# Optimization experiments

Hardware: AMD Instinct MI355X
Metric: run time of the kernel (lower is better)

Reference implementation:

```python
import jax, jax.numpy as jnp
import numpy as np

DIM = 384
HEADS = 12
HEAD_DIM = DIM // HEADS
WS = 8
SHIFT = 4
HID = int(DIM * 4.0)
N = WS * WS
EPS = 1e-5
NEG = -1e9


def _rel_index(ws):
    coords = np.stack(np.meshgrid(np.arange(ws), np.arange(ws), indexing='ij')).reshape(2, -1)
    rel = (coords[:, :, None] - coords[:, None, :]).transpose(1, 2, 0)
    rel[:, :, 0] += ws - 1
    rel[:, :, 1] += ws - 1
    return (rel[:, :, 0] * (2 * ws - 1) + rel[:, :, 1]).astype(np.int32)

REL_IDX = _rel_index(WS)  # [N, N]


def _shift_mask(H, W, ws, shift):
    img = np.zeros((H, W))
    cnt = 0
    sl = (slice(0, -ws), slice(-ws, -shift), slice(-shift, None))
    for h in sl:
        for w in sl:
            img[h, w] = cnt
            cnt += 1
    m = img.reshape(H // ws, ws, W // ws, ws).transpose(0, 2, 1, 3).reshape(-1, ws * ws)
    diff = m[:, :, None] - m[:, None, :]
    return np.where(diff != 0, NEG, 0.0).astype(np.float32)  # [nW, N, N]


def _ln(x, g, b):
    mu = jnp.mean(x, axis=-1, keepdims=True)
    var = jnp.mean(jnp.square(x - mu), axis=-1, keepdims=True)
    return (x - mu) * jax.lax.rsqrt(var + EPS) * g + b


def _l2norm(x):
    n = jnp.sqrt(jnp.sum(jnp.square(x), axis=-1, keepdims=True))
    return x / jnp.maximum(n, 1e-12)


def setup_inputs() -> dict:
    key = jax.random.key(0)
    ks = jax.random.split(key, 12)
    s = 0.02
    return {
        'x': jax.random.normal(ks[0], (16, 4096, DIM), jnp.float32),
        'H': 64,
        'W': 64,
        'norm_attn_g': jnp.ones((DIM,), jnp.float32),
        'norm_attn_b': jnp.zeros((DIM,), jnp.float32),
        'qkv_w': jax.random.normal(ks[1], (DIM, 3 * DIM), jnp.float32) * s,
        'qkv_b': jnp.zeros((3 * DIM,), jnp.float32),
        'proj_w': jax.random.normal(ks[2], (DIM, DIM), jnp.float32) * s,
        'proj_b': jnp.zeros((DIM,), jnp.float32),
        'tau': jnp.full((HEADS,), 0.07, jnp.float32),
        'rpb_table': jax.random.normal(ks[3], ((2 * WS - 1) ** 2, HEADS), jnp.float32) * s,
        'norm_mlp_g': jnp.ones((DIM,), jnp.float32),
        'norm_mlp_b': jnp.zeros((DIM,), jnp.float32),
        'fc1_w': jax.random.normal(ks[4], (DIM, HID), jnp.float32) * s,
        'fc1_b': jnp.zeros((HID,), jnp.float32),
        'fc2_w': jax.random.normal(ks[5], (HID, DIM), jnp.float32) * s,
        'fc2_b': jnp.zeros((DIM,), jnp.float32),
    }


def reference(x, H, W, norm_attn_g, norm_attn_b, qkv_w, qkv_b, proj_w, proj_b, tau,
              rpb_table, norm_mlp_g, norm_mlp_b, fc1_w, fc1_b, fc2_w, fc2_b):
    B, L, C = x.shape
    ws = WS
    nW = (H // ws) * (W // ws)
    mask = jnp.asarray(_shift_mask(H, W, ws, SHIFT))  # [nW, N, N], static

    shortcut = x
    xn = _ln(x, norm_attn_g, norm_attn_b).reshape(B, H, W, C)
    xn = jnp.roll(xn, (-SHIFT, -SHIFT), axis=(1, 2))
    # window partition -> [B*nW, N, C]
    win = xn.reshape(B, H // ws, ws, W // ws, ws, C).transpose(0, 1, 3, 2, 4, 5).reshape(-1, N, C)
    BnW = win.shape[0]

    qkv = (win @ qkv_w + qkv_b).reshape(BnW, N, 3, HEADS, HEAD_DIM)
    q = _l2norm(qkv[:, :, 0])  # [BnW, N, H, D]
    k = _l2norm(qkv[:, :, 1])
    v = qkv[:, :, 2]

    attn = jnp.einsum('bnhd,bmhd->bhnm', q, k)
    attn = attn / jnp.clip(tau, 0.001)[None, :, None, None]
    bias = rpb_table[REL_IDX.reshape(-1)].reshape(N, N, HEADS).transpose(2, 0, 1)  # [H, N, N]
    attn = attn + bias[None]
    attn = attn.reshape(B, nW, HEADS, N, N) + mask[None, :, None]
    attn = jax.nn.softmax(attn.reshape(BnW, HEADS, N, N), axis=-1)

    out = jnp.einsum('bhnm,bmhd->bnhd', attn, v).reshape(BnW, N, C)
    out = out @ proj_w + proj_b
    # window unpartition
    out = out.reshape(B, H // ws, W // ws, ws, ws, C).transpose(0, 1, 3, 2, 4, 5).reshape(B, H, W, C)
    out = jnp.roll(out, (SHIFT, SHIFT), axis=(1, 2)).reshape(B, L, C)

    x = shortcut + out
    xn2 = _ln(x, norm_mlp_g, norm_mlp_b)
    mlp = jax.nn.gelu(xn2 @ fc1_w + fc1_b, approximate=False) @ fc2_w + fc2_b
    return x + mlp
```

## Files before the change

### kernel.cpp

```cpp
#include <hip/hip_runtime.h>
#include <hip/hip_bf16.h>
#include <cstdint>

#define DIM     384
#define NHEADS  12
#define HD      32
#define HGRID   64
#define NTOK    64
#define MTOT    65536
#define HID     1536

typedef __attribute__((ext_vector_type(8))) short bf16x8;
typedef __attribute__((ext_vector_type(4))) float f32x4;
typedef __hip_bfloat16 bf16;

typedef __attribute__((address_space(1))) const void* as1_cvp;
typedef __attribute__((address_space(3))) void*       as3_vp;
#define GLDS16(g, l) __builtin_amdgcn_global_load_lds((as1_cvp)(g), (as3_vp)(l), 16, 0, 0)

__device__ __forceinline__ float bf2f(short s) {
  union { unsigned int u; float f; } x;
  x.u = ((unsigned int)(unsigned short)s) << 16;
  return x.f;
}
__device__ __forceinline__ unsigned int f2u(float f) {
  union { bf16 b; unsigned short s; } c;
  c.b = __float2bfloat16(f);
  return (unsigned int)c.s;
}

__global__ void wconv_kernel(const float* __restrict__ src, bf16* __restrict__ dst,
                             int K, int N) {
  int i = blockIdx.x * 256 + threadIdx.x;
  if (i >= K * N) return;
  int n = i / K, k = i - n * K;
  dst[i] = __float2bfloat16(src[(size_t)k * N + n]);
}

__global__ __launch_bounds__(384) void ln_kernel(const float* __restrict__ x,
    const float* __restrict__ g, const float* __restrict__ bta,
    bf16* __restrict__ out, int windowed) {
  const int row = blockIdx.x;
  const int c = threadIdx.x;
  size_t src;
  if (windowed) {
    int wg = row >> 6, n = row & 63;
    int b = wg >> 6, wi = wg & 63;
    int hp = ((wi >> 3) << 3) + (n >> 3);
    int wp = ((wi & 7) << 3) + (n & 7);
    int h = (hp + 4) & 63, w = (wp + 4) & 63;
    src = ((size_t)b * 4096 + h * 64 + w) * DIM;
  } else {
    src = (size_t)row * DIM;
  }
  float v = x[src + c];
  float s = v, ss = v * v;
  #pragma unroll
  for (int off = 32; off; off >>= 1) {
    s  += __shfl_xor(s,  off, 64);
    ss += __shfl_xor(ss, off, 64);
  }
  __shared__ float red[12];
  const int wave = threadIdx.x >> 6, lane = threadIdx.x & 63;
  if (lane == 0) { red[wave] = s; red[6 + wave] = ss; }
  __syncthreads();
  if (threadIdx.x == 0) {
    float ts = 0.f, tss = 0.f;
    #pragma unroll
    for (int i = 0; i < 6; i++) { ts += red[i]; tss += red[6 + i]; }
    red[0] = ts; red[6] = tss;
  }
  __syncthreads();
  const float mean = red[0] * (1.0f / DIM);
  const float var  = red[6] * (1.0f / DIM) - mean * mean;
  const float inv  = rsqrtf(var + 1e-5f);
  out[(size_t)row * DIM + c] = __float2bfloat16((v - mean) * inv * g[c] + bta[c]);
}

template <int EPI>
__global__ __launch_bounds__(512) void gemm_bt(
    const bf16* __restrict__ A, const bf16* __restrict__ Bt,
    const float* __restrict__ bias,
    bf16* __restrict__ outb, float* __restrict__ outf,
    const float* __restrict__ resid,
    int M, int N, int K, int gridN)
{
  __shared__ bf16 As[2][128 * 64];
  __shared__ bf16 Bs[2][128 * 64];
  const int tid = threadIdx.x;
  const int wave = tid >> 6, lane = tid & 63;

  const int bid = blockIdx.x;
  const int xcd = bid & 7, slot = bid >> 3;
  const int n_blk = slot % gridN;
  const int m_blk = (slot / gridN) * 8 + xcd;
  const int m0 = m_blk * 128, n0 = n_blk * 128;

  f32x4 acc[4][2];
  #pragma unroll
  for (int i = 0; i < 4; i++)
    #pragma unroll
    for (int j = 0; j < 2; j++) acc[i][j] = (f32x4){0.f, 0.f, 0.f, 0.f};

  const int q = lane >> 4, r = lane & 15;
  const int mwav = (wave >> 2) * 64;
  const int nwav = (wave & 3) * 32;

  const int srow = wave * 16 + (lane >> 3);
  const int gchunk = (lane & 7) ^ ((lane >> 3) & 7);
  const char* Ac = (const char*)A + (size_t)(m0 + srow) * K * 2 + gchunk * 16;
  const char* Bc = (const char*)Bt + (size_t)(n0 + srow) * K * 2 + gchunk * 16;
  const size_t rowskip8 = (size_t)8 * K * 2;
  const int ldsbase = wave * 16 * 64;

  const int rxor = r & 7;
  const int nt = K >> 6;

  {
    bf16* Ad = &As[0][ldsbase];
    bf16* Bd = &Bs[0][ldsbase];
    GLDS16(Ac,            Ad + 0 * 64);
    GLDS16(Ac + rowskip8, Ad + 8 * 64);
    GLDS16(Bc,            Bd + 0 * 64);
    GLDS16(Bc + rowskip8, Bd + 8 * 64);
  }

  int cur = 0;
  for (int t = 0; t < nt; ++t) {
    if (t + 1 < nt) {
      const size_t kb = (size_t)(t + 1) * 128;
      bf16* Ad = &As[cur ^ 1][ldsbase];
      bf16* Bd = &Bs[cur ^ 1][ldsbase];
      GLDS16(Ac + kb,            Ad + 0 * 64);
      GLDS16(Ac + kb + rowskip8, Ad + 8 * 64);
      GLDS16(Bc + kb,            Bd + 0 * 64);
      GLDS16(Bc + kb + rowskip8, Bd + 8 * 64);
      asm volatile("s_waitcnt vmcnt(4)" ::: "memory");
    } else {
      asm volatile("s_waitcnt vmcnt(0)" ::: "memory");
    }
    __builtin_amdgcn_sched_barrier(0);
    __builtin_amdgcn_s_barrier();

    const bf16* Ar = As[cur];
    const bf16* Br = Bs[cur];
    #pragma unroll
    for (int hh = 0; hh < 2; hh++) {
      const int s = (hh * 4 + q) ^ rxor;
      bf16x8 af[4], bfr[2];
      #pragma unroll
      for (int mi = 0; mi < 4; mi++)
        af[mi] = *(const bf16x8*)(&Ar[(mwav + mi * 16 + r) * 64 + s * 8]);
      #pragma unroll
      for (int ni = 0; ni < 2; ni++)
        bfr[ni] = *(const bf16x8*)(&Br[(nwav + ni * 16 + r) * 64 + s * 8]);
      #pragma unroll
      for (int mi = 0; mi < 4; mi++)
        #pragma unroll
        for (int ni = 0; ni < 2; ni++)
          acc[mi][ni] = __builtin_amdgcn_mfma_f32_16x16x32_bf16(af[mi], bfr[ni], acc[mi][ni], 0, 0, 0);
    }

    __builtin_amdgcn_s_barrier();
    cur ^= 1;
  }

  #pragma unroll
  for (int mi = 0; mi < 4; mi++) {
    #pragma unroll
    for (int ni = 0; ni < 2; ni++) {
      #pragma unroll
      for (int rr = 0; rr < 4; rr++) {
        const int row = m0 + mwav + mi * 16 + q * 4 + rr;
        const int col = n0 + nwav + ni * 16 + r;
        float val = acc[mi][ni][rr] + bias[col];
        if (EPI == 0) {
          outb[(size_t)row * N + col] = __float2bfloat16(val);
        } else if (EPI == 1) {
          const float t = val * val;
          const float z = val * fmaf(t, 0.07135481283f, 1.5957691216f);
          const float gl = val / (1.0f + __expf(-z));
          outb[(size_t)row * N + col] = __float2bfloat16(gl);
        } else if (EPI == 2) {
          const int wg = row >> 6, n = row & 63;
          const int b = wg >> 6, wi = wg & 63;
          const int hp = ((wi >> 3) << 3) + (n >> 3);
          const int wp = ((wi & 7) << 3) + (n & 7);
          const int h = (hp + 4) & 63, w = (wp + 4) & 63;
          const size_t dst = ((size_t)b * 4096 + h * 64 + w) * DIM + col;
          outf[dst] = resid[dst] + val;
        } else {
          outf[(size_t)row * N + col] += val;
        }
      }
    }
  }
}

__device__ __forceinline__ int regid(int v) { return v < 56 ? 0 : (v < 60 ? 1 : 2); }

__global__ __launch_bounds__(256, 2) void attn_kernel(
    const bf16* __restrict__ qkv, const float* __restrict__ tau,
    const float* __restrict__ rpb, bf16* __restrict__ outb)
{
  const int wv = threadIdx.x >> 6;
  const int lane = threadIdx.x & 63;
  const int q4 = lane >> 4, r = lane & 15;
  const int h = blockIdx.x * 4 + wv;
  const int w = blockIdx.y;

  __shared__ bf16  pbuf[4][64 * 64];
  __shared__ float rpb_s[4][228];
  __shared__ float kscs[4][64];

  for (int t = lane; t < 225; t += 64)
    rpb_s[wv][t] = rpb[t * NHEADS + h];

  const size_t rowbase = ((size_t)w * 64) * 1152 + (size_t)h * 32;
  bf16x8 qf[4], kf[4];
  #pragma unroll
  for (int mi = 0; mi < 4; mi++) {
    const size_t ro = rowbase + (size_t)(mi * 16 + r) * 1152 + q4 * 8;
    qf[mi] = *(const bf16x8*)(qkv + ro);
    kf[mi] = *(const bf16x8*)(qkv + ro + 384);
  }

  const bf16* vbase = qkv + rowbase + 768;
  unsigned short vraw[2][2][8];
  #pragma unroll
  for (int ks = 0; ks < 2; ks++)
    #pragma unroll
    for (int nd = 0; nd < 2; nd++)
      #pragma unroll
      for (int t = 0; t < 8; t++)
        vraw[ks][nd][t] = *(const unsigned short*)(vbase +
            (size_t)(ks * 32 + q4 * 8 + t) * 1152 + nd * 16 + r);

  float qsc[4];
  {
    const float tinv = 1.0f / fmaxf(tau[h], 1e-3f);
    #pragma unroll
    for (int mi = 0; mi < 4; mi++) {
      float sq = 0.f, sk = 0.f;
      #pragma unroll
      for (int e = 0; e < 8; e++) {
        float a = bf2f(qf[mi][e]), b = bf2f(kf[mi][e]);
        sq = fmaf(a, a, sq); sk = fmaf(b, b, sk);
      }
      sq += __shfl_xor(sq, 16, 64); sq += __shfl_xor(sq, 32, 64);
      sk += __shfl_xor(sk, 16, 64); sk += __shfl_xor(sk, 32, 64);
      qsc[mi] = tinv / fmaxf(sqrtf(sq), 1e-12f);
      if (q4 == 0) kscs[wv][mi * 16 + r] = 1.0f / fmaxf(sqrtf(sk), 1e-12f);
    }
  }

  f32x4 sacc[4][4];
  #pragma unroll
  for (int a = 0; a < 4; a++)
    #pragma unroll
    for (int b = 0; b < 4; b++) sacc[a][b] = (f32x4){0.f, 0.f, 0.f, 0.f};
  #pragma unroll
  for (int mj = 0; mj < 4; mj++)
    #pragma unroll
    for (int mi = 0; mi < 4; mi++)
      sacc[mj][mi] = __builtin_amdgcn_mfma_f32_16x16x32_bf16(kf[mj], qf[mi], sacc[mj][mi], 0, 0, 0);

  const int wi = w & 63, wy = wi >> 3, wx = wi & 7;
  int byi[4], regi[4];
  #pragma unroll
  for (int mi = 0; mi < 4; mi++) {
    const int i = mi * 16 + r, iy = i >> 3, ix = i & 7;
    byi[mi]  = (iy + 7) * 15 + (ix + 7);
    regi[mi] = regid(wy * 8 + iy) * 3 + regid(wx * 8 + ix);
  }
  float kscv[4][4];
  #pragma unroll
  for (int mj = 0; mj < 4; mj++)
    #pragma unroll
    for (int reg = 0; reg < 4; reg++)
      kscv[mj][reg] = kscs[wv][mj * 16 + q4 * 4 + reg];

  float mx[4] = {-3e38f, -3e38f, -3e38f, -3e38f};
  #pragma unroll
  for (int mj = 0; mj < 4; mj++) {
    #pragma unroll
    for (int reg = 0; reg < 4; reg++) {
      const int j = mj * 16 + q4 * 4 + reg;
      const int jy = j >> 3, jx = j & 7;
      const int offj = jy * 15 + jx;
      const int regj = regid(wy * 8 + jy) * 3 + regid(wx * 8 + jx);
      const float kv = kscv[mj][reg];
      #pragma unroll
      for (int mi = 0; mi < 4; mi++) {
        float v = sacc[mj][mi][reg] * (qsc[mi] * kv) + rpb_s[wv][byi[mi] - offj];
        if (regj != regi[mi]) v -= 1e9f;
        sacc[mj][mi][reg] = v;
        mx[mi] = fmaxf(mx[mi], v);
      }
    }
  }
  float sum[4] = {0.f, 0.f, 0.f, 0.f};
  #pragma unroll
  for (int mi = 0; mi < 4; mi++) {
    mx[mi] = fmaxf(mx[mi], __shfl_xor(mx[mi], 16, 64));
    mx[mi] = fmaxf(mx[mi], __shfl_xor(mx[mi], 32, 64));
  }
  #pragma unroll
  for (int mj = 0; mj < 4; mj++)
    #pragma unroll
    for (int mi = 0; mi < 4; mi++)
      #pragma unroll
      for (int reg = 0; reg < 4; reg++) {
        float p = __expf(sacc[mj][mi][reg] - mx[mi]);
        sacc[mj][mi][reg] = p;
        sum[mi] += p;
      }
  float rinv[4];
  #pragma unroll
  for (int mi = 0; mi < 4; mi++) {
    sum[mi] += __shfl_xor(sum[mi], 16, 64);
    sum[mi] += __shfl_xor(sum[mi], 32, 64);
    rinv[mi] = 1.0f / sum[mi];
  }

  #pragma unroll
  for (int mj = 0; mj < 4; mj++) {
    #pragma unroll
    for (int mi = 0; mi < 4; mi++) {
      const int i = mi * 16 + r;
      const int cs = (mj * 4 + q4) ^ r;
      uint2 d;
      d.x = f2u(sacc[mj][mi][0] * rinv[mi]) | (f2u(sacc[mj][mi][1] * rinv[mi]) << 16);
      d.y = f2u(sacc[mj][mi][2] * rinv[mi]) | (f2u(sacc[mj][mi][3] * rinv[mi]) << 16);
      *(uint2*)(&pbuf[wv][i * 64 + cs * 4]) = d;
    }
  }

  bf16x8 vf[2][2];
  #pragma unroll
  for (int ks = 0; ks < 2; ks++)
    #pragma unroll
    for (int nd = 0; nd < 2; nd++) {
      union { unsigned int u[4]; bf16x8 v; } t;
      #pragma unroll
      for (int e = 0; e < 4; e++)
        t.u[e] = (unsigned int)vraw[ks][nd][2 * e] |
                 ((unsigned int)vraw[ks][nd][2 * e + 1] << 16);
      vf[ks][nd] = t.v;
    }

  f32x4 oacc[4][2];
  #pragma unroll
  for (int a = 0; a < 4; a++)
    #pragma unroll
    for (int b = 0; b < 2; b++) oacc[a][b] = (f32x4){0.f, 0.f, 0.f, 0.f};
  #pragma unroll
  for (int mi = 0; mi < 4; mi++) {
    const int i = mi * 16 + r;
    #pragma unroll
    for (int ks = 0; ks < 2; ks++) {
      const int c1 = (ks * 8 + q4 * 2) ^ r;
      const int c2 = (ks * 8 + q4 * 2 + 1) ^ r;
      union { unsigned int u[4]; bf16x8 v; } pf;
      uint2 lo = *(const uint2*)(&pbuf[wv][i * 64 + c1 * 4]);
      uint2 hi = *(const uint2*)(&pbuf[wv][i * 64 + c2 * 4]);
      pf.u[0] = lo.x; pf.u[1] = lo.y; pf.u[2] = hi.x; pf.u[3] = hi.y;
      #pragma unroll
      for (int nd = 0; nd < 2; nd++)
        oacc[mi][nd] = __builtin_amdgcn_mfma_f32_16x16x32_bf16(pf.v, vf[ks][nd], oacc[mi][nd], 0, 0, 0);
    }
  }

  #pragma unroll
  for (int mi = 0; mi < 4; mi++)
    #pragma unroll
    for (int nd = 0; nd < 2; nd++)
      #pragma unroll
      for (int reg = 0; reg < 4; reg++) {
        const int i = mi * 16 + q4 * 4 + reg;
        outb[((size_t)w * 64 + i) * DIM + h * 32 + nd * 16 + r] =
            __float2bfloat16(oacc[mi][nd][reg]);
      }
}

extern "C" void kernel_launch(void* const* d_in, const int* in_sizes, int n_in,
                              void* d_out, int out_size, void* d_ws, size_t ws_size,
                              hipStream_t stream) {
  const float* x      = (const float*)d_in[0];
  const float* ln1_g  = (const float*)d_in[3];
  const float* ln1_b  = (const float*)d_in[4];
  const float* qkv_w  = (const float*)d_in[5];
  const float* qkv_b  = (const float*)d_in[6];
  const float* proj_w = (const float*)d_in[7];
  const float* proj_b = (const float*)d_in[8];
  const float* tau    = (const float*)d_in[9];
  const float* rpb    = (const float*)d_in[10];
  const float* ln2_g  = (const float*)d_in[11];
  const float* ln2_b  = (const float*)d_in[12];
  const float* fc1_w  = (const float*)d_in[13];
  const float* fc1_b  = (const float*)d_in[14];
  const float* fc2_w  = (const float*)d_in[15];
  const float* fc2_b  = (const float*)d_in[16];
  float* out = (float*)d_out;
  char* ws = (char*)d_ws;

  bf16* wT_qkv  = (bf16*)(ws + 0);
  bf16* wT_proj = (bf16*)(ws + 884736);
  bf16* wT_fc1  = (bf16*)(ws + 1179648);
  bf16* wT_fc2  = (bf16*)(ws + 2359296);
  bf16* winb    = (bf16*)(ws + 4194304);
  bf16* qkvb    = (bf16*)(ws + 54525952);
  bf16* attnb   = (bf16*)(ws + 205520896);
  bf16* xn2b    = winb;
  bf16* hb      = qkvb;

  wconv_kernel<<<(384 * 1152 + 255) / 256, 256, 0, stream>>>(qkv_w, wT_qkv, 384, 1152);
  wconv_kernel<<<(384 * 384 + 255) / 256, 256, 0, stream>>>(proj_w, wT_proj, 384, 384);
  wconv_kernel<<<(384 * 1536 + 255) / 256, 256, 0, stream>>>(fc1_w, wT_fc1, 384, 1536);
  wconv_kernel<<<(1536 * 384 + 255) / 256, 256, 0, stream>>>(fc2_w, wT_fc2, 1536, 384);

  ln_kernel<<<MTOT, 384, 0, stream>>>(x, ln1_g, ln1_b, winb, 1);
  gemm_bt<0><<<(MTOT / 128) * (1152 / 128), 512, 0, stream>>>(
      winb, wT_qkv, qkv_b, qkvb, nullptr, nullptr, MTOT, 1152, 384, 1152 / 128);
  attn_kernel<<<dim3(3, 1024), 256, 0, stream>>>(qkvb, tau, rpb, attnb);
  gemm_bt<2><<<(MTOT / 128) * (384 / 128), 512, 0, stream>>>(
      attnb, wT_proj, proj_b, nullptr, out, x, MTOT, 384, 384, 384 / 128);
  ln_kernel<<<MTOT, 384, 0, stream>>>(out, ln2_g, ln2_b, xn2b, 0);
  gemm_bt<1><<<(MTOT / 128) * (HID / 128), 512, 0, stream>>>(
      xn2b, wT_fc1, fc1_b, hb, nullptr, nullptr, MTOT, HID, 384, HID / 128);
  gemm_bt<3><<<(MTOT / 128) * (384 / 128), 512, 0, stream>>>(
      hb, wT_fc2, fc2_b, nullptr, out, nullptr, MTOT, 384, HID, 384 / 128);
}
```

Measured before the change: 840.2 us.

## Use wave-per-row LayerNorm and fuse residual add into second LayerNorm

LayerNorm kernels now process one row per wavefront, with six elements per lane and shuffle-only reductions, replacing the 384-thread block that synchronised through shared memory. The projection GEMM now writes bf16 output in window order. A new kernel gathers that output back to image order, adds the residual, writes x and computes LN2 in one pass. This removes the scattered fp32 read-modify-write in the GEMM epilogue and a separate read of the fp32 output for LN2. The trade-off is an extra bf16 intermediate and the rounding of the projection output to bf16 before the residual add.

New measurement: 711.9 us. -15.3%, faster.

```diff
diff --git a/kernel.cpp b/kernel.cpp
--- a/kernel.cpp
+++ b/kernel.cpp
@@ -28,6 +28,11 @@
   c.b = __float2bfloat16(f);
   return (unsigned int)c.s;
 }
+__device__ __forceinline__ unsigned short f2us(float f) {
+  union { bf16 b; unsigned short s; } c;
+  c.b = __float2bfloat16(f);
+  return c.s;
+}
 
 __global__ void wconv_kernel(const float* __restrict__ src, bf16* __restrict__ dst,
                              int K, int N) {
@@ -37,44 +42,106 @@
   dst[i] = __float2bfloat16(src[(size_t)k * N + n]);
 }
 
-__global__ __launch_bounds__(384) void ln_kernel(const float* __restrict__ x,
+__global__ __launch_bounds__(256) void ln1_kernel(const float* __restrict__ x,
     const float* __restrict__ g, const float* __restrict__ bta,
-    bf16* __restrict__ out, int windowed) {
-  const int row = blockIdx.x;
-  const int c = threadIdx.x;
-  size_t src;
-  if (windowed) {
-    int wg = row >> 6, n = row & 63;
-    int b = wg >> 6, wi = wg & 63;
-    int hp = ((wi >> 3) << 3) + (n >> 3);
-    int wp = ((wi & 7) << 3) + (n & 7);
-    int h = (hp + 4) & 63, w = (wp + 4) & 63;
-    src = ((size_t)b * 4096 + h * 64 + w) * DIM;
-  } else {
-    src = (size_t)row * DIM;
-  }
-  float v = x[src + c];
-  float s = v, ss = v * v;
+    bf16* __restrict__ out) {
+  const int row = blockIdx.x * 4 + (threadIdx.x >> 6);
+  const int lane = threadIdx.x & 63;
+  const int c0 = lane * 6;
+
+  const int wg = row >> 6, n = row & 63;
+  const int b = wg >> 6, wi = wg & 63;
+  const int hp = ((wi >> 3) << 3) + (n >> 3);
+  const int wp = ((wi & 7) << 3) + (n & 7);
+  const int h = (hp + 4) & 63, w = (wp + 4) & 63;
+  const float* xr = x + ((size_t)b * 4096 + h * 64 + w) * DIM + c0;
+
+  float v[6];
+  {
+    float2 a0 = *(const float2*)(xr);
+    float2 a1 = *(const float2*)(xr + 2);
+    float2 a2 = *(const float2*)(xr + 4);
+    v[0] = a0.x; v[1] = a0.y; v[2] = a1.x; v[3] = a1.y; v[4] = a2.x; v[5] = a2.y;
+  }
+  float s = 0.f, ss = 0.f;
+  #pragma unroll
+  for (int i = 0; i < 6; i++) { s += v[i]; ss = fmaf(v[i], v[i], ss); }
   #pragma unroll
   for (int off = 32; off; off >>= 1) {
     s  += __shfl_xor(s,  off, 64);
     ss += __shfl_xor(ss, off, 64);
   }
-  __shared__ float red[12];
-  const int wave = threadIdx.x >> 6, lane = threadIdx.x & 63;
-  if (lane == 0) { red[wave] = s; red[6 + wave] = ss; }
-  __syncthreads();
-  if (threadIdx.x == 0) {
-    float ts = 0.f, tss = 0.f;
-    #pragma unroll
-    for (int i = 0; i < 6; i++) { ts += red[i]; tss += red[6 + i]; }
-    red[0] = ts; red[6] = tss;
-  }
-  __syncthreads();
-  const float mean = red[0] * (1.0f / DIM);
-  const float var  = red[6] * (1.0f / DIM) - mean * mean;
+  const float mean = s * (1.0f / DIM);
+  const float var  = ss * (1.0f / DIM) - mean * mean;
   const float inv  = rsqrtf(var + 1e-5f);
-  out[(size_t)row * DIM + c] = __float2bfloat16((v - mean) * inv * g[c] + bta[c]);
+
+  const float* gp = g + c0;
+  const float* bp = bta + c0;
+  unsigned short o[6];
+  #pragma unroll
+  for (int i = 0; i < 6; i++)
+    o[i] = f2us((v[i] - mean) * inv * gp[i] + bp[i]);
+  bf16* op = out + (size_t)row * DIM + c0;
+  *(ushort2*)(op)     = make_ushort2(o[0], o[1]);
+  *(ushort2*)(op + 2) = make_ushort2(o[2], o[3]);
+  *(ushort2*)(op + 4) = make_ushort2(o[4], o[5]);
+}
+
+__global__ __launch_bounds__(256) void resid_ln2_kernel(const float* __restrict__ x,
+    const bf16* __restrict__ projb,
+    const float* __restrict__ g, const float* __restrict__ bta,
+    float* __restrict__ out, bf16* __restrict__ xn2) {
+  const int row = blockIdx.x * 4 + (threadIdx.x >> 6);
+  const int lane = threadIdx.x & 63;
+  const int c0 = lane * 6;
+
+  const int b = row >> 12, r12 = row & 4095;
+  const int hh = r12 >> 6, ww = r12 & 63;
+  const int hp = (hh + 60) & 63, wp = (ww + 60) & 63;
+  const int wi = ((hp >> 3) << 3) + (wp >> 3);
+  const int n  = ((hp & 7) << 3) + (wp & 7);
+  const bf16* pr = projb + ((size_t)b * 4096 + wi * 64 + n) * DIM + c0;
+  const float* xr = x + (size_t)row * DIM + c0;
+
+  float v[6];
+  {
+    float2 a0 = *(const float2*)(xr);
+    float2 a1 = *(const float2*)(xr + 2);
+    float2 a2 = *(const float2*)(xr + 4);
+    ushort2 p0 = *(const ushort2*)(pr);
+    ushort2 p1 = *(const ushort2*)(pr + 2);
+    ushort2 p2 = *(const ushort2*)(pr + 4);
+    v[0] = a0.x + bf2f(p0.x); v[1] = a0.y + bf2f(p0.y);
+    v[2] = a1.x + bf2f(p1.x); v[3] = a1.y + bf2f(p1.y);
+    v[4] = a2.x + bf2f(p2.x); v[5] = a2.y + bf2f(p2.y);
+  }
+  float* orow = out + (size_t)row * DIM + c0;
+  *(float2*)(orow)     = make_float2(v[0], v[1]);
+  *(float2*)(orow + 2) = make_float2(v[2], v[3]);
+  *(float2*)(orow + 4) = make_float2(v[4], v[5]);
+
+  float s = 0.f, ss = 0.f;
+  #pragma unroll
+  for (int i = 0; i < 6; i++) { s += v[i]; ss = fmaf(v[i], v[i], ss); }
+  #pragma unroll
+  for (int off = 32; off; off >>= 1) {
+    s  += __shfl_xor(s,  off, 64);
+    ss += __shfl_xor(ss, off, 64);
+  }
+  const float mean = s * (1.0f / DIM);
+  const float var  = ss * (1.0f / DIM) - mean * mean;
+  const float inv  = rsqrtf(var + 1e-5f);
+
+  const float* gp = g + c0;
+  const float* bp = bta + c0;
+  unsigned short o[6];
+  #pragma unroll
+  for (int i = 0; i < 6; i++)
+    o[i] = f2us((v[i] - mean) * inv * gp[i] + bp[i]);
+  bf16* op = xn2 + (size_t)row * DIM + c0;
+  *(ushort2*)(op)     = make_ushort2(o[0], o[1]);
+  *(ushort2*)(op + 2) = make_ushort2(o[2], o[3]);
+  *(ushort2*)(op + 4) = make_ushort2(o[4], o[5]);
 }
 
 template <int EPI>
@@ -181,14 +248,6 @@
           const float z = val * fmaf(t, 0.07135481283f, 1.5957691216f);
           const float gl = val / (1.0f + __expf(-z));
           outb[(size_t)row * N + col] = __float2bfloat16(gl);
-        } else if (EPI == 2) {
-          const int wg = row >> 6, n = row & 63;
-          const int b = wg >> 6, wi = wg & 63;
-          const int hp = ((wi >> 3) << 3) + (n >> 3);
-          const int wp = ((wi & 7) << 3) + (n & 7);
-          const int h = (hp + 4) & 63, w = (wp + 4) & 63;
-          const size_t dst = ((size_t)b * 4096 + h * 64 + w) * DIM + col;
-          outf[dst] = resid[dst] + val;
         } else {
           outf[(size_t)row * N + col] += val;
         }
@@ -412,6 +471,7 @@
   bf16* qkvb    = (bf16*)(ws + 54525952);
   bf16* attnb   = (bf16*)(ws + 205520896);
   bf16* xn2b    = winb;
+  bf16* projb   = qkvb;
   bf16* hb      = qkvb;
 
   wconv_kernel<<<(384 * 1152 + 255) / 256, 256, 0, stream>>>(qkv_w, wT_qkv, 384, 1152);
@@ -419,13 +479,13 @@
   wconv_kernel<<<(384 * 1536 + 255) / 256, 256, 0, stream>>>(fc1_w, wT_fc1, 384, 1536);
   wconv_kernel<<<(1536 * 384 + 255) / 256, 256, 0, stream>>>(fc2_w, wT_fc2, 1536, 384);
 
-  ln_kernel<<<MTOT, 384, 0, stream>>>(x, ln1_g, ln1_b, winb, 1);
+  ln1_kernel<<<MTOT / 4, 256, 0, stream>>>(x, ln1_g, ln1_b, winb);
   gemm_bt<0><<<(MTOT / 128) * (1152 / 128), 512, 0, stream>>>(
       winb, wT_qkv, qkv_b, qkvb, nullptr, nullptr, MTOT, 1152, 384, 1152 / 128);
   attn_kernel<<<dim3(3, 1024), 256, 0, stream>>>(qkvb, tau, rpb, attnb);
-  gemm_bt<2><<<(MTOT / 128) * (384 / 128), 512, 0, stream>>>(
-      attnb, wT_proj, proj_b, nullptr, out, x, MTOT, 384, 384, 384 / 128);
-  ln_kernel<<<MTOT, 384, 0, stream>>>(out, ln2_g, ln2_b, xn2b, 0);
+  gemm_bt<0><<<(MTOT / 128) * (384 / 128), 512, 0, stream>>>(
+      attnb, wT_proj, proj_b, projb, nullptr, nullptr, MTOT, 384, 384, 384 / 128);
+  resid_ln2_kernel<<<MTOT / 4, 256, 0, stream>>>(x, projb, ln2_g, ln2_b, out, xn2b);
   gemm_bt<1><<<(MTOT / 128) * (HID / 128), 512, 0, stream>>>(
       xn2b, wT_fc1, fc1_b, hb, nullptr, nullptr, MTOT, HID, 384, HID / 128);
   gemm_bt<3><<<(MTOT / 128) * (384 / 128), 512, 0, stream>>>(
```
